# Performance work log

Measured on AMD Instinct MI355X. Metric: run time of the kernel, lower is better.

## Reference

```python
import jax, jax.numpy as jnp
import numpy as np

K = 4  # top-k nearest neighbors


def setup_inputs() -> dict:
    key = jax.random.key(0)
    k1, k2, k3 = jax.random.split(key, 3)
    N, D, M = 784, 512, 65536  # N_patches (28*28), feature dim, memory bank size
    query = jax.random.normal(k1, (N, D), dtype=jnp.float32)
    memory_bank = jax.random.normal(k2, (M, D), dtype=jnp.float32)
    # fcn: Conv2d(in=2*D=1024, out=1, kernel=3, padding=1)
    fan_in = 2 * D * 9
    fcn_w = jax.random.normal(k3, (1, 2 * D, 3, 3), dtype=jnp.float32) / np.sqrt(fan_in)
    fcn_b = jnp.zeros((1,), dtype=jnp.float32)
    return {"query": query, "memory_bank": memory_bank, "fcn_w": fcn_w, "fcn_b": fcn_b}


def reference(query, memory_bank, fcn_w, fcn_b):
    # pairwise L2 distances (torch.cdist p=2): [N, M]
    q2 = jnp.sum(query * query, axis=1, keepdims=True)           # [N, 1]
    m2 = jnp.sum(memory_bank * memory_bank, axis=1)              # [M]
    d2 = q2 + m2[None, :] - 2.0 * (query @ memory_bank.T)        # [N, M]
    dist = jnp.sqrt(jnp.maximum(d2, 0.0))
    # top-k smallest distances -> indices
    _, topk_idx = jax.lax.top_k(-dist, K)                        # [N, K]
    neighbors = memory_bank[topk_idx]                            # [N, K, D] gather
    neighbor_mean = jnp.mean(neighbors, axis=1)                  # [N, D]
    combined = jnp.concatenate([query, neighbor_mean], axis=1)   # [N, 2D]
    n, dim = combined.shape
    s = int(np.sqrt(n))                                          # 28
    x = combined.T.reshape(1, dim, s, s)                         # [1, 2D, 28, 28]
    out = jax.lax.conv_general_dilated(
        x, fcn_w, window_strides=(1, 1), padding=((1, 1), (1, 1)),
        dimension_numbers=("NCHW", "OIHW", "NCHW"))
    return out + fcn_b[None, :, None, None]                      # [1, 1, 28, 28]
```

## Files before the change

kernel.cpp:

```cpp
#include <hip/hip_runtime.h>
#include <hip/hip_fp8.h>
#include <stdint.h>

#define DIMS 512
#define NQ 784
#define QPAD 832
#define NTILE 13
#define RESCORE 32
#define CSTR 528
#define TBYTES (64 * CSTR)

typedef float f32x4 __attribute__((ext_vector_type(4)));
typedef long  l2v  __attribute__((ext_vector_type(2)));

__device__ __forceinline__ unsigned umn(unsigned a, unsigned b) { return a < b ? a : b; }
__device__ __forceinline__ unsigned umx(unsigned a, unsigned b) { return a > b ? a : b; }

__device__ __forceinline__ unsigned pk4(float a, float b, float c, float d) {
#if __has_builtin(__builtin_amdgcn_cvt_pk_fp8_f32)
    int v = 0;
    v = __builtin_amdgcn_cvt_pk_fp8_f32(a, b, v, false);
    v = __builtin_amdgcn_cvt_pk_fp8_f32(c, d, v, true);
    return (unsigned)v;
#else
    __hip_fp8_e4m3 x(a), y(b), z(c), w(d);
    return (unsigned)x.__x | ((unsigned)y.__x << 8) | ((unsigned)z.__x << 16) | ((unsigned)w.__x << 24);
#endif
}

__global__ __launch_bounds__(256) void prep_query(const float* __restrict__ q,
                                                  char* __restrict__ qb8p) {
    int gid = blockIdx.x * 256 + threadIdx.x;
    int col = gid >> 6;
    int g = gid & 63;
    float4 a = make_float4(0.f, 0.f, 0.f, 0.f), b = a;
    if (col < NQ) {
        a = *(const float4*)(q + (size_t)col * DIMS + g * 8);
        b = *(const float4*)(q + (size_t)col * DIMS + g * 8 + 4);
    }
    uint2 o;
    o.x = pk4(a.x, a.y, a.z, a.w);
    o.y = pk4(b.x, b.y, b.z, b.w);
    int tile = col >> 6, cin = col & 63;
    *(uint2*)(qb8p + (size_t)tile * TBYTES + cin * CSTR + (g & 3) * 128 + (g >> 2) * 8) = o;
}

__global__ __launch_bounds__(512, 1) void score_kernel(
    const float* __restrict__ bank,
    const char* __restrict__ qb8p,
    uint2* __restrict__ cand)
{
    __shared__ __align__(16) char bt[4][TBYTES];
    __shared__ float m2s[256];

    const int wg = blockIdx.x;
    const int t = threadIdx.x;
    const int v = t >> 6;
    const int lane = t & 63;
    const int lo = lane & 15;
    const int kg = lane >> 4;

#define STAGE(BUF, TILE)                                                                   \
    do {                                                                                   \
        if (v == 7) {                                                                      \
            const char* s32 = qb8p + (size_t)(TILE) * TBYTES + 32 * 1024 + lane * 16;      \
            __builtin_amdgcn_global_load_lds(                                              \
                (const __attribute__((address_space(1))) unsigned*)s32,                    \
                (__attribute__((address_space(3))) unsigned*)(&bt[0][0] + (size_t)(BUF) * TBYTES + 32 * 1024), \
                16, 0, 0);                                                                 \
        }                                                                                  \
        _Pragma("unroll")                                                                  \
        for (int j = 0; j < 4; ++j) {                                                      \
            const int ch = v * 4 + j;                                                      \
            const char* src = qb8p + (size_t)(TILE) * TBYTES + ch * 1024 + lane * 16;      \
            __builtin_amdgcn_global_load_lds(                                              \
                (const __attribute__((address_space(1))) unsigned*)src,                    \
                (__attribute__((address_space(3))) unsigned*)(&bt[0][0] + (size_t)(BUF) * TBYTES + ch * 1024), \
                16, 0, 0);                                                                 \
        }                                                                                  \
    } while (0)

    STAGE(0, 0);
    STAGE(1, 1);
    STAGE(2, 2);

    long areg[2][16];
    #pragma unroll
    for (int m = 0; m < 2; ++m) {
        const float* rp = bank + ((size_t)(wg * 256 + v * 32 + m * 16 + lo)) * DIMS + kg * 8;
        float ss = 0.f;
        #pragma unroll
        for (int ks = 0; ks < 16; ++ks) {
            float4 x = *(const float4*)(rp + ks * 32);
            float4 y = *(const float4*)(rp + ks * 32 + 4);
            ss += x.x * x.x + x.y * x.y + x.z * x.z + x.w * x.w;
            ss += y.x * y.x + y.y * y.y + y.z * y.z + y.w * y.w;
            unsigned l32 = pk4(x.x, x.y, x.z, x.w);
            unsigned h32 = pk4(y.x, y.y, y.z, y.w);
            areg[m][ks] = (long)(((unsigned long long)h32 << 32) | l32);
        }
        ss += __shfl_xor(ss, 16);
        ss += __shfl_xor(ss, 32);
        if (lane < 16) m2s[v * 32 + m * 16 + lane] = ss;
    }

    f32x4 seed[2];
    #pragma unroll
    for (int m = 0; m < 2; ++m)
        #pragma unroll
        for (int j = 0; j < 4; ++j)
            seed[m][j] = -(512.0f + 0.5f * m2s[v * 32 + m * 16 + kg * 4 + j]);

    const char* pB = &bt[0][0] + lo * CSTR + kg * 128;

#define LOADB(DST, PBT, KS2)                                       \
    do {                                                           \
        DST##0 = *(const l2v*)((PBT) + 0 * 8448 + (KS2) * 16);     \
        DST##1 = *(const l2v*)((PBT) + 1 * 8448 + (KS2) * 16);     \
        DST##2 = *(const l2v*)((PBT) + 2 * 8448 + (KS2) * 16);     \
        DST##3 = *(const l2v*)((PBT) + 3 * 8448 + (KS2) * 16);     \
    } while (0)

#define MFMAS(B, KS2)                                                                            \
    do {                                                                                         \
        acc[0][0] = __builtin_amdgcn_mfma_f32_16x16x32_fp8_fp8(areg[0][2*(KS2)], B##0[0], acc[0][0], 0, 0, 0); \
        acc[1][0] = __builtin_amdgcn_mfma_f32_16x16x32_fp8_fp8(areg[1][2*(KS2)], B##0[0], acc[1][0], 0, 0, 0); \
        acc[0][1] = __builtin_amdgcn_mfma_f32_16x16x32_fp8_fp8(areg[0][2*(KS2)], B##1[0], acc[0][1], 0, 0, 0); \
        acc[1][1] = __builtin_amdgcn_mfma_f32_16x16x32_fp8_fp8(areg[1][2*(KS2)], B##1[0], acc[1][1], 0, 0, 0); \
        acc[0][2] = __builtin_amdgcn_mfma_f32_16x16x32_fp8_fp8(areg[0][2*(KS2)], B##2[0], acc[0][2], 0, 0, 0); \
        acc[1][2] = __builtin_amdgcn_mfma_f32_16x16x32_fp8_fp8(areg[1][2*(KS2)], B##2[0], acc[1][2], 0, 0, 0); \
        acc[0][3] = __builtin_amdgcn_mfma_f32_16x16x32_fp8_fp8(areg[0][2*(KS2)], B##3[0], acc[0][3], 0, 0, 0); \
        acc[1][3] = __builtin_amdgcn_mfma_f32_16x16x32_fp8_fp8(areg[1][2*(KS2)], B##3[0], acc[1][3], 0, 0, 0); \
        acc[0][0] = __builtin_amdgcn_mfma_f32_16x16x32_fp8_fp8(areg[0][2*(KS2)+1], B##0[1], acc[0][0], 0, 0, 0); \
        acc[1][0] = __builtin_amdgcn_mfma_f32_16x16x32_fp8_fp8(areg[1][2*(KS2)+1], B##0[1], acc[1][0], 0, 0, 0); \
        acc[0][1] = __builtin_amdgcn_mfma_f32_16x16x32_fp8_fp8(areg[0][2*(KS2)+1], B##1[1], acc[0][1], 0, 0, 0); \
        acc[1][1] = __builtin_amdgcn_mfma_f32_16x16x32_fp8_fp8(areg[1][2*(KS2)+1], B##1[1], acc[1][1], 0, 0, 0); \
        acc[0][2] = __builtin_amdgcn_mfma_f32_16x16x32_fp8_fp8(areg[0][2*(KS2)+1], B##2[1], acc[0][2], 0, 0, 0); \
        acc[1][2] = __builtin_amdgcn_mfma_f32_16x16x32_fp8_fp8(areg[1][2*(KS2)+1], B##2[1], acc[1][2], 0, 0, 0); \
        acc[0][3] = __builtin_amdgcn_mfma_f32_16x16x32_fp8_fp8(areg[0][2*(KS2)+1], B##3[1], acc[0][3], 0, 0, 0); \
        acc[1][3] = __builtin_amdgcn_mfma_f32_16x16x32_fp8_fp8(areg[1][2*(KS2)+1], B##3[1], acc[1][3], 0, 0, 0); \
    } while (0)

#define SELT(T)                                                                            \
    do {                                                                                   \
        _Pragma("unroll")                                                                  \
        for (int n = 0; n < 4; ++n) {                                                      \
            unsigned v1 = 0xFFFFFFFFu, v2 = 0xFFFFFFFFu;                                   \
            _Pragma("unroll")                                                              \
            for (int m = 0; m < 2; ++m)                                                    \
                _Pragma("unroll")                                                          \
                for (int j = 0; j < 4; ++j) {                                              \
                    unsigned u = ((__float_as_uint(acc[m][n][j]) ^ 0x80000000u) & ~31u)    \
                                 | (unsigned)(m * 16 + kg * 4 + j);                        \
                    unsigned mx = umx(v1, u);                                              \
                    v1 = umn(v1, u);                                                       \
                    v2 = umn(v2, mx);                                                      \
                }                                                                          \
            _Pragma("unroll")                                                              \
            for (int off = 16; off <= 32; off <<= 1) {                                     \
                unsigned o1 = (unsigned)__shfl_xor((int)v1, off);                          \
                unsigned o2 = (unsigned)__shfl_xor((int)v2, off);                          \
                unsigned mx = umx(v1, o1);                                                 \
                v1 = umn(v1, o1);                                                          \
                v2 = umn(umn(v2, o2), mx);                                                 \
            }                                                                              \
            int col = (T) * 64 + n * 16 + lo;                                              \
            if (lane < 16 && col < NQ)                                                     \
                cand[(size_t)(wg * 8 + v) * QPAD + col] = make_uint2(v1, v2);              \
        }                                                                                  \
    } while (0)

#define COMPUTE(T)                                                                         \
    do {                                                                                   \
        const char* pBt = pB + (size_t)((T) & 3) * TBYTES;                                 \
        f32x4 acc[2][4];                                                                   \
        _Pragma("unroll")                                                                  \
        for (int m = 0; m < 2; ++m)                                                        \
            _Pragma("unroll")                                                              \
            for (int n = 0; n < 4; ++n) acc[m][n] = seed[m];                               \
        l2v Ba0, Ba1, Ba2, Ba3, Bb0, Bb1, Bb2, Bb3;                                        \
        LOADB(Ba, pBt, 0);                                                                 \
        __builtin_amdgcn_s_setprio(1);                                                     \
        LOADB(Bb, pBt, 1); MFMAS(Ba, 0);                                                   \
        LOADB(Ba, pBt, 2); MFMAS(Bb, 1);                                                   \
        LOADB(Bb, pBt, 3); MFMAS(Ba, 2);                                                   \
        LOADB(Ba, pBt, 4); MFMAS(Bb, 3);                                                   \
        LOADB(Bb, pBt, 5); MFMAS(Ba, 4);                                                   \
        LOADB(Ba, pBt, 6); MFMAS(Bb, 5);                                                   \
        LOADB(Bb, pBt, 7); MFMAS(Ba, 6);                                                   \
        MFMAS(Bb, 7);                                                                      \
        __builtin_amdgcn_s_setprio(0);                                                     \
        SELT(T);                                                                           \
    } while (0)

#define WAITV(N) asm volatile("s_waitcnt vmcnt(" #N ")" ::: "memory")

    #pragma unroll 1
    for (int tile = 0; tile < 10; ++tile) {
        WAITV(8);
        __builtin_amdgcn_s_barrier();
        STAGE((tile + 3) & 3, tile + 3);
        COMPUTE(tile);
    }
    WAITV(8);  __builtin_amdgcn_s_barrier();  COMPUTE(10);
    WAITV(4);  __builtin_amdgcn_s_barrier();  COMPUTE(11);
    WAITV(0);  __builtin_amdgcn_s_barrier();  COMPUTE(12);

#undef WAITV
#undef COMPUTE
#undef SELT
#undef MFMAS
#undef LOADB
#undef STAGE
}

__global__ __launch_bounds__(256) void merge_kernel(
    const float* __restrict__ query, const float* __restrict__ bank,
    const uint2* __restrict__ cand, float* __restrict__ nm)
{
    __shared__ double d2s[4][32];
    __shared__ int    cis[4][32];

    const int wv = threadIdx.x >> 6, lane = threadIdx.x & 63;
    const int row = blockIdx.x * 4 + wv;

    unsigned s0 = ~0u, s1 = ~0u, s2 = ~0u, s3 = ~0u;
    unsigned s4 = ~0u, s5 = ~0u, s6 = ~0u, s7 = ~0u;

#define INS(U)                                        \
    do {                                              \
        unsigned tt = (U), nv;                        \
        nv = umn(s0, tt); tt = umx(s0, tt); s0 = nv;  \
        nv = umn(s1, tt); tt = umx(s1, tt); s1 = nv;  \
        nv = umn(s2, tt); tt = umx(s2, tt); s2 = nv;  \
        nv = umn(s3, tt); tt = umx(s3, tt); s3 = nv;  \
        nv = umn(s4, tt); tt = umx(s4, tt); s4 = nv;  \
        nv = umn(s5, tt); tt = umx(s5, tt); s5 = nv;  \
        nv = umn(s6, tt); tt = umx(s6, tt); s6 = nv;  \
        s7 = umn(s7, tt);                             \
    } while (0)

    #pragma unroll 4
    for (int j = 0; j < 32; ++j) {
        uint2 e = cand[((size_t)(lane * 32 + j)) * QPAD + row];
        unsigned jb = (unsigned)(j << 5);
        INS((e.x & ~0x3E0u) | jb);
        INS((e.y & ~0x3E0u) | jb);
    }
#undef INS

    const int myC = lane & 31;
    int myCand = 0;
    #pragma unroll
    for (int it = 0; it < RESCORE; ++it) {
        unsigned gm = s0;
        #pragma unroll
        for (int off = 1; off < 64; off <<= 1)
            gm = umn(gm, (unsigned)__shfl_xor((int)gm, off));
        unsigned long long bal = __ballot(s0 == gm);
        int wl = __ffsll((long long)bal) - 1;
        int ci = (wl * 32 + (int)((gm >> 5) & 31u)) * 32 + (int)(gm & 31u);
        myCand = (it == myC) ? ci : myCand;
        if (lane == wl) { s0 = s1; s1 = s2; s2 = s3; s3 = s4; s4 = s5; s5 = s6; s6 = s7; s7 = ~0u; }
    }

    const float* qr = query + (size_t)row * DIMS + (lane >> 5) * 256;
    const float* mr = bank + (size_t)myCand * DIMS + (lane >> 5) * 256;
    double s = 0.0;
    #pragma unroll 8
    for (int i = 0; i < 64; ++i) {
        float4 a = *(const float4*)(qr + i * 4);
        float4 b = *(const float4*)(mr + i * 4);
        double d;
        d = (double)a.x - (double)b.x; s += d * d;
        d = (double)a.y - (double)b.y; s += d * d;
        d = (double)a.z - (double)b.z; s += d * d;
        d = (double)a.w - (double)b.w; s += d * d;
    }
    s += __shfl_xor(s, 32);
    if (lane < 32) { d2s[wv][lane] = s; cis[wv][lane] = myCand; }
    __syncthreads();

    int sel0 = 0, sel1 = 0, sel2 = 0, sel3 = 0;
    unsigned used = 0;
    #pragma unroll
    for (int k = 0; k < 4; ++k) {
        double bv = 1e300; int bidx = 0x7FFFFFFF; int bc = 0;
        for (int c = 0; c < 32; ++c) {
            bool live = !((used >> c) & 1u);
            double dv = d2s[wv][c];
            int cv = cis[wv][c];
            if (live && (dv < bv || (dv == bv && cv < bidx))) { bv = dv; bidx = cv; bc = c; }
        }
        used |= 1u << bc;
        if (k == 0) sel0 = bidx; else if (k == 1) sel1 = bidx;
        else if (k == 2) sel2 = bidx; else sel3 = bidx;
    }

    const float* r0 = bank + (size_t)sel0 * DIMS + lane * 8;
    const float* r1 = bank + (size_t)sel1 * DIMS + lane * 8;
    const float* r2 = bank + (size_t)sel2 * DIMS + lane * 8;
    const float* r3 = bank + (size_t)sel3 * DIMS + lane * 8;
    float* dst = nm + (size_t)row * DIMS + lane * 8;
    #pragma unroll
    for (int h = 0; h < 2; ++h) {
        float4 a = *(const float4*)(r0 + h * 4);
        float4 b = *(const float4*)(r1 + h * 4);
        float4 c = *(const float4*)(r2 + h * 4);
        float4 d = *(const float4*)(r3 + h * 4);
        float4 o;
        o.x = 0.25f * (a.x + b.x + c.x + d.x);
        o.y = 0.25f * (a.y + b.y + c.y + d.y);
        o.z = 0.25f * (a.z + b.z + c.z + d.z);
        o.w = 0.25f * (a.w + b.w + c.w + d.w);
        *(float4*)(dst + h * 4) = o;
    }
}

__global__ __launch_bounds__(256) void conv_kernel(
    const float* __restrict__ query, const float* __restrict__ nm,
    const float* __restrict__ fw, const float* __restrict__ fb,
    float* __restrict__ out)
{
    __shared__ float red[256];
    int pix = blockIdx.x, t = threadIdx.x;
    int i = pix / 28, j = pix % 28;
    float acc = 0.f;
    for (int c = t; c < 1024; c += 256) {
        const float* wrow = fw + c * 9;
        for (int di = 0; di < 3; ++di) {
            int h = i + di - 1;
            if (h < 0 || h >= 28) continue;
            for (int dj = 0; dj < 3; ++dj) {
                int w = j + dj - 1;
                if (w < 0 || w >= 28) continue;
                int n = h * 28 + w;
                float x = (c < 512) ? query[(size_t)n * 512 + c]
                                    : nm[(size_t)n * 512 + (c - 512)];
                acc += x * wrow[di * 3 + dj];
            }
        }
    }
    red[t] = acc;
    __syncthreads();
    for (int s = 128; s; s >>= 1) {
        if (t < s) red[t] += red[t + s];
        __syncthreads();
    }
    if (t == 0) out[pix] = red[0] + fb[0];
}

extern "C" void kernel_launch(void* const* d_in, const int* in_sizes, int n_in,
                              void* d_out, int out_size, void* d_ws, size_t ws_size,
                              hipStream_t stream)
{
    const float* query = (const float*)d_in[0];
    const float* bank  = (const float*)d_in[1];
    const float* fw    = (const float*)d_in[2];
    const float* fb    = (const float*)d_in[3];
    float* out = (float*)d_out;

    char* ws = (char*)d_ws;
    char*  qb8p = ws;
    uint2* cand = (uint2*)(ws + 439296);
    float* nm   = (float*)(ws + 439296 + 13631488);

    prep_query<<<208, 256, 0, stream>>>(query, qb8p);
    score_kernel<<<256, 512, 0, stream>>>(bank, qb8p, cand);
    merge_kernel<<<NQ / 4, 256, 0, stream>>>(query, bank, cand, nm);
    conv_kernel<<<NQ, 256, 0, stream>>>(query, nm, fw, fb, out);
}
```

Baseline: 121.0 us.

## Split bank FP8 conversion into a prep kernel and shrink score workgroups

Moves the fp32-to-fp8 conversion and squared-norm computation of the memory bank into a separate prep_bank kernel. The score kernel now loads pre-packed fp8 rows and launches 512 blocks of 256 threads with double-buffered query tiles instead of 256 blocks of 512 threads with quad buffering. The candidate array is transposed to a row-major per-query layout so the merge kernel reads contiguously. This raises occupancy (two blocks per CU) and cuts bank read bytes in the score kernel, but adds a full extra pass over the bank plus a write and read of a 32 MB fp8 copy, and reduces prefetch depth.

```diff
diff --git a/kernel.cpp b/kernel.cpp
--- a/kernel.cpp
+++ b/kernel.cpp
@@ -6,6 +6,7 @@
 #define NQ 784
 #define QPAD 832
 #define NTILE 13
+#define NGROUP 2048
 #define RESCORE 32
 #define CSTR 528
 #define TBYTES (64 * CSTR)
@@ -45,13 +46,33 @@
     *(uint2*)(qb8p + (size_t)tile * TBYTES + cin * CSTR + (g & 3) * 128 + (g >> 2) * 8) = o;
 }
 
-__global__ __launch_bounds__(512, 1) void score_kernel(
-    const float* __restrict__ bank,
+__global__ __launch_bounds__(256) void prep_bank(const float* __restrict__ bank,
+                                                 char* __restrict__ bank8,
+                                                 float* __restrict__ m2) {
+    const int row = blockIdx.x * 4 + (threadIdx.x >> 6);
+    const int lane = threadIdx.x & 63;
+    const float* rp = bank + (size_t)row * DIMS + lane * 8;
+    float4 a = *(const float4*)rp;
+    float4 b = *(const float4*)(rp + 4);
+    float ss = a.x * a.x + a.y * a.y + a.z * a.z + a.w * a.w
+             + b.x * b.x + b.y * b.y + b.z * b.z + b.w * b.w;
+    #pragma unroll
+    for (int off = 1; off < 64; off <<= 1) ss += __shfl_xor(ss, off);
+    if (lane == 0) m2[row] = ss;
+    uint2 o;
+    o.x = pk4(a.x, a.y, a.z, a.w);
+    o.y = pk4(b.x, b.y, b.z, b.w);
+    *(uint2*)(bank8 + (size_t)row * DIMS + lane * 8) = o;
+}
+
+__global__ __launch_bounds__(256, 2) void score_kernel(
+    const char* __restrict__ bank8,
+    const float* __restrict__ m2g,
     const char* __restrict__ qb8p,
     uint2* __restrict__ cand)
 {
-    __shared__ __align__(16) char bt[4][TBYTES];
-    __shared__ float m2s[256];
+    __shared__ __align__(16) char bt[2][TBYTES];
+    __shared__ float m2Ls[128];
 
     const int wg = blockIdx.x;
     const int t = threadIdx.x;
@@ -60,56 +81,39 @@
     const int lo = lane & 15;
     const int kg = lane >> 4;
 
-#define STAGE(BUF, TILE)                                                                   \
-    do {                                                                                   \
-        if (v == 7) {                                                                      \
-            const char* s32 = qb8p + (size_t)(TILE) * TBYTES + 32 * 1024 + lane * 16;      \
-            __builtin_amdgcn_global_load_lds(                                              \
-                (const __attribute__((address_space(1))) unsigned*)s32,                    \
-                (__attribute__((address_space(3))) unsigned*)(&bt[0][0] + (size_t)(BUF) * TBYTES + 32 * 1024), \
-                16, 0, 0);                                                                 \
-        }                                                                                  \
-        _Pragma("unroll")                                                                  \
-        for (int j = 0; j < 4; ++j) {                                                      \
-            const int ch = v * 4 + j;                                                      \
-            const char* src = qb8p + (size_t)(TILE) * TBYTES + ch * 1024 + lane * 16;      \
-            __builtin_amdgcn_global_load_lds(                                              \
-                (const __attribute__((address_space(1))) unsigned*)src,                    \
+#define STAGE(BUF, TILE)                                                              \
+    do {                                                                              \
+        _Pragma("unroll")                                                             \
+        for (int j = 0; j < 9; ++j) {                                                 \
+            const int ch = (j < 8) ? (v * 8 + j) : 32;                                \
+            const char* src = qb8p + (size_t)(TILE) * TBYTES + ch * 1024 + lane * 16; \
+            __builtin_amdgcn_global_load_lds(                                         \
+                (const __attribute__((address_space(1))) unsigned*)src,               \
                 (__attribute__((address_space(3))) unsigned*)(&bt[0][0] + (size_t)(BUF) * TBYTES + ch * 1024), \
-                16, 0, 0);                                                                 \
-        }                                                                                  \
+                16, 0, 0);                                                            \
+        }                                                                             \
     } while (0)
 
     STAGE(0, 0);
-    STAGE(1, 1);
-    STAGE(2, 2);
 
     long areg[2][16];
-    #pragma unroll
-    for (int m = 0; m < 2; ++m) {
-        const float* rp = bank + ((size_t)(wg * 256 + v * 32 + m * 16 + lo)) * DIMS + kg * 8;
-        float ss = 0.f;
+    {
+        const char* ab = bank8 + ((size_t)(wg * 128 + v * 32 + lo)) * DIMS + kg * 8;
         #pragma unroll
-        for (int ks = 0; ks < 16; ++ks) {
-            float4 x = *(const float4*)(rp + ks * 32);
-            float4 y = *(const float4*)(rp + ks * 32 + 4);
-            ss += x.x * x.x + x.y * x.y + x.z * x.z + x.w * x.w;
-            ss += y.x * y.x + y.y * y.y + y.z * y.z + y.w * y.w;
-            unsigned l32 = pk4(x.x, x.y, x.z, x.w);
-            unsigned h32 = pk4(y.x, y.y, y.z, y.w);
-            areg[m][ks] = (long)(((unsigned long long)h32 << 32) | l32);
-        }
-        ss += __shfl_xor(ss, 16);
-        ss += __shfl_xor(ss, 32);
-        if (lane < 16) m2s[v * 32 + m * 16 + lane] = ss;
-    }
+        for (int m = 0; m < 2; ++m)
+            #pragma unroll
+            for (int ks = 0; ks < 16; ++ks)
+                areg[m][ks] = *(const long*)(ab + m * (16 * DIMS) + ks * 32);
+    }
+    if (t < 128) m2Ls[t] = m2g[wg * 128 + t];
+    __syncthreads();
 
     f32x4 seed[2];
     #pragma unroll
     for (int m = 0; m < 2; ++m)
         #pragma unroll
         for (int j = 0; j < 4; ++j)
-            seed[m][j] = -(512.0f + 0.5f * m2s[v * 32 + m * 16 + kg * 4 + j]);
+            seed[m][j] = -(512.0f + 0.5f * m2Ls[v * 32 + m * 16 + kg * 4 + j]);
 
     const char* pB = &bt[0][0] + lo * CSTR + kg * 128;
 
@@ -166,13 +170,13 @@
             }                                                                              \
             int col = (T) * 64 + n * 16 + lo;                                              \
             if (lane < 16 && col < NQ)                                                     \
-                cand[(size_t)(wg * 8 + v) * QPAD + col] = make_uint2(v1, v2);              \
+                cand[(size_t)col * NGROUP + (wg * 4 + v)] = make_uint2(v1, v2);            \
         }                                                                                  \
     } while (0)
 
 #define COMPUTE(T)                                                                         \
     do {                                                                                   \
-        const char* pBt = pB + (size_t)((T) & 3) * TBYTES;                                 \
+        const char* pBt = pB + (size_t)((T) & 1) * TBYTES;                                 \
         f32x4 acc[2][4];                                                                   \
         _Pragma("unroll")                                                                  \
         for (int m = 0; m < 2; ++m)                                                        \
@@ -193,20 +197,14 @@
         SELT(T);                                                                           \
     } while (0)
 
-#define WAITV(N) asm volatile("s_waitcnt vmcnt(" #N ")" ::: "memory")
-
     #pragma unroll 1
-    for (int tile = 0; tile < 10; ++tile) {
-        WAITV(8);
+    for (int tile = 0; tile < NTILE; ++tile) {
+        asm volatile("s_waitcnt vmcnt(4)" ::: "memory");
         __builtin_amdgcn_s_barrier();
-        STAGE((tile + 3) & 3, tile + 3);
+        if (tile + 1 < NTILE) STAGE((tile + 1) & 1, tile + 1);
         COMPUTE(tile);
     }
-    WAITV(8);  __builtin_amdgcn_s_barrier();  COMPUTE(10);
-    WAITV(4);  __builtin_amdgcn_s_barrier();  COMPUTE(11);
-    WAITV(0);  __builtin_amdgcn_s_barrier();  COMPUTE(12);
-
-#undef WAITV
+
 #undef COMPUTE
 #undef SELT
 #undef MFMAS
@@ -240,9 +238,10 @@
         s7 = umn(s7, tt);                             \
     } while (0)
 
+    const uint2* crow = cand + (size_t)row * NGROUP + lane * 32;
     #pragma unroll 4
     for (int j = 0; j < 32; ++j) {
-        uint2 e = cand[((size_t)(lane * 32 + j)) * QPAD + row];
+        uint2 e = crow[j];
         unsigned jb = (unsigned)(j << 5);
         INS((e.x & ~0x3E0u) | jb);
         INS((e.y & ~0x3E0u) | jb);
@@ -361,12 +360,15 @@
     float* out = (float*)d_out;
 
     char* ws = (char*)d_ws;
-    char*  qb8p = ws;
-    uint2* cand = (uint2*)(ws + 439296);
-    float* nm   = (float*)(ws + 439296 + 13631488);
+    char*  qb8p  = ws;
+    char*  bank8 = ws + 439296;
+    float* m2    = (float*)(ws + 33993728);
+    uint2* cand  = (uint2*)(ws + 34255872);
+    float* nm    = (float*)(ws + 47887360);
 
     prep_query<<<208, 256, 0, stream>>>(query, qb8p);
-    score_kernel<<<256, 512, 0, stream>>>(bank, qb8p, cand);
+    prep_bank<<<16384, 256, 0, stream>>>(bank, bank8, m2);
+    score_kernel<<<512, 256, 0, stream>>>(bank8, m2, qb8p, cand);
     merge_kernel<<<NQ / 4, 256, 0, stream>>>(query, bank, cand, nm);
     conv_kernel<<<NQ, 256, 0, stream>>>(query, nm, fw, fb, out);
 }
```

Result: no change. 121.3 us (+0.2%).
